# Kernel tuning notes

Hardware: AMD Instinct MI355X
Metric: run time of the kernel (lower is better)

The kernel has to match this reference:

```python
import jax, jax.numpy as jnp
import numpy as np

B, T, C = 2, 2048, 1024
E = 1024          # total attention embedding (head_size arg of TransformerBlock)
H = 16            # n_heads
HS = E // H       # per-head size = 64
FF = 4 * C        # ffwd_mul * in_embd
EPS = 1e-5


def setup_inputs() -> dict:
    key = jax.random.key(0)
    ks = jax.random.split(key, 20)
    s = lambda fan_in: 1.0 / np.sqrt(fan_in)
    return {
        "x":     jax.random.normal(ks[0], (B, T, C), jnp.float32),
        "Wq":    jax.random.normal(ks[1], (C, E), jnp.float32) * s(C),
        "bq":    jnp.zeros((E,), jnp.float32),
        "Wk":    jax.random.normal(ks[2], (C, E), jnp.float32) * s(C),
        "bk":    jnp.zeros((E,), jnp.float32),
        "Wv":    jax.random.normal(ks[3], (C, E), jnp.float32) * s(C),
        "bv":    jnp.zeros((E,), jnp.float32),
        "Wo":    jax.random.normal(ks[4], (E, C), jnp.float32) * s(E),
        "bo":    jnp.zeros((C,), jnp.float32),
        "ln1_g": jnp.ones((C,), jnp.float32),
        "ln1_b": jnp.zeros((C,), jnp.float32),
        "W1":    jax.random.normal(ks[5], (C, FF), jnp.float32) * s(C),
        "b1":    jnp.zeros((FF,), jnp.float32),
        "W2":    jax.random.normal(ks[6], (FF, C), jnp.float32) * s(FF),
        "b2":    jnp.zeros((C,), jnp.float32),
        "ln2_g": jnp.ones((C,), jnp.float32),
        "ln2_b": jnp.zeros((C,), jnp.float32),
        "Wc":    jax.random.normal(ks[7], (C, C), jnp.float32) * s(C),
        "bc":    jnp.zeros((C,), jnp.float32),
    }


def _layernorm(x, g, b):
    mu = jnp.mean(x, axis=-1, keepdims=True)
    var = jnp.mean(jnp.square(x - mu), axis=-1, keepdims=True)
    return (x - mu) * jax.lax.rsqrt(var + EPS) * g + b


def _attention(x, Wq, bq, Wk, bk, Wv, bv, Wo, bo):
    # batched equivalent of the per-head Linear q/k/v loop + concat
    q = (x @ Wq + bq).reshape(B, T, H, HS)
    k = (x @ Wk + bk).reshape(B, T, H, HS)
    v = (x @ Wv + bv).reshape(B, T, H, HS)
    scores = jnp.einsum("bthd,bshd->bhts", q, k) / np.sqrt(HS)  # no causal mask in source
    wei = jax.nn.softmax(scores, axis=-1)
    out = jnp.einsum("bhts,bshd->bthd", wei, v).reshape(B, T, E)
    return out @ Wo + bo


def reference(x, Wq, bq, Wk, bk, Wv, bv, Wo, bo, ln1_g, ln1_b,
              W1, b1, W2, b2, ln2_g, ln2_b, Wc, bc):
    out = _layernorm(x + _attention(x, Wq, bq, Wk, bk, Wv, bv, Wo, bo), ln1_g, ln1_b)
    ff = jax.nn.gelu(out @ W1 + b1, approximate=False) @ W2 + b2  # torch GELU is exact erf
    out = _layernorm(out + ff, ln2_g, ln2_b)
    # Conv1d(C, C, kernel_size=1) over transposed input == pointwise linear
    out = out @ Wc.T + bc
    return out
```

## Files before the change

kernel.cpp:

```cpp
#include <hip/hip_runtime.h>
#include <hip/hip_bf16.h>
#include <cstdint>
#include <cstddef>

#define DEVINL __device__ __forceinline__

typedef __attribute__((ext_vector_type(4)))  float f32x4;
typedef __attribute__((ext_vector_type(16))) float f32x16;
typedef __attribute__((ext_vector_type(8)))  short s16x8;

#define QSCALE 0.1803368801111204f

DEVINL short f2bf(float f) {
  union { float f; unsigned u; } v; v.f = f;
  unsigned r = (v.u + 0x7fffu + ((v.u >> 16) & 1u)) >> 16;
  return (short)r;
}

DEVINL void gload_lds16(const void* g, void* l) {
  __builtin_amdgcn_global_load_lds((const __attribute__((address_space(1))) void*)g,
                                   (__attribute__((address_space(3))) void*)l,
                                   16, 0, 0);
}

DEVINL s16x8 lds_frag(const short* base, int row, int cb) {
  const int addr = row * 128 + (cb ^ ((row & 7) << 4));
  return *(const s16x8*)((const char*)base + addr);
}

enum { EPI_F32 = 0, EPI_GELU = 1, EPI_RES = 2, EPI_QKV = 3 };

template <int EPI, int BM>
__global__ __launch_bounds__(256) void gemm_bt(
    const short* __restrict__ A, const short* __restrict__ Bt,
    const float* __restrict__ bias, const float* __restrict__ res,
    float* __restrict__ outF, short* __restrict__ outB,
    short* __restrict__ qp, short* __restrict__ kp, short* __restrict__ vt,
    int M, int N, int K)
{
  constexpr int MI = BM / 32;
  constexpr int CAW = BM / 64;
  __shared__ short As[2][BM * 32];
  __shared__ short Bs[2][128 * 32];
  const int tid = threadIdx.x;
  const int w = tid >> 6, lane = tid & 63;
  const int wr = w >> 1, wc = w & 1;

  const int gx = gridDim.x;
  int id = blockIdx.x + gx * blockIdx.y;
  const int cpx = (gx * gridDim.y) >> 3;
  id = (id & 7) * cpx + (id >> 3);
  const int n0 = (id % gx) * 128, m0 = (id / gx) * BM;

  const int lrow = lane >> 2, lk = (lane & 3) << 3;
  const short* Ag = A + (size_t)m0 * K;
  const short* Bg = Bt + (size_t)n0 * K;

#define GSTAGE(kk, bufi)                                                     \
  {                                                                          \
    _Pragma("unroll") for (int i = 0; i < CAW; ++i) {                        \
      const int c = w * CAW + i;                                             \
      gload_lds16(Ag + (size_t)(c * 16 + lrow) * K + ((kk) + lk),            \
                  &As[bufi][c * 512]);                                       \
    }                                                                        \
    _Pragma("unroll") for (int i = 0; i < 2; ++i) {                          \
      const int c = w * 2 + i;                                               \
      gload_lds16(Bg + (size_t)(c * 16 + lrow) * K + ((kk) + lk),            \
                  &Bs[bufi][c * 512]);                                       \
    }                                                                        \
  }

  f32x4 acc[MI][4] = {};

  GSTAGE(0, 0);
  __syncthreads();
  int cur = 0;

  for (int kk = 0; kk < K; kk += 32) {
    if (kk + 32 < K) GSTAGE(kk + 32, cur ^ 1);
    s16x8 af[MI], bf[4];
#pragma unroll
    for (int mi = 0; mi < MI; ++mi)
      af[mi] = *(const s16x8*)&As[cur][(wr * (BM / 2) + mi * 16 + (lane & 15)) * 32 + ((lane >> 4) << 3)];
#pragma unroll
    for (int ni = 0; ni < 4; ++ni)
      bf[ni] = *(const s16x8*)&Bs[cur][(wc * 64 + ni * 16 + (lane & 15)) * 32 + ((lane >> 4) << 3)];
    __builtin_amdgcn_s_setprio(1);
#pragma unroll
    for (int mi = 0; mi < MI; ++mi)
#pragma unroll
      for (int ni = 0; ni < 4; ++ni)
        acc[mi][ni] = __builtin_amdgcn_mfma_f32_16x16x32_bf16(af[mi], bf[ni], acc[mi][ni], 0, 0, 0);
    __builtin_amdgcn_s_setprio(0);
    __syncthreads();
    cur ^= 1;
  }
#undef GSTAGE

  const int rbase = m0 + wr * (BM / 2) + ((lane >> 4) << 2);
  const int cbase = n0 + wc * 64 + (lane & 15);
#pragma unroll
  for (int mi = 0; mi < MI; ++mi) {
#pragma unroll
    for (int ni = 0; ni < 4; ++ni) {
      const int col = cbase + ni * 16;
      const float bv = bias[col];
      if (EPI == EPI_QKV) {
        const int e = col & 1023, id3 = col >> 10;
        const int h = e >> 6, d = e & 63;
        const int row0 = rbase + mi * 16;
        const int b = row0 >> 11, t0 = row0 & 2047;
        if (id3 == 0) {
#pragma unroll
          for (int j = 0; j < 4; ++j)
            qp[((size_t)(b * 16 + h) * 2048 + t0 + j) * 64 + d] = f2bf((acc[mi][ni][j] + bv) * QSCALE);
        } else if (id3 == 1) {
#pragma unroll
          for (int j = 0; j < 4; ++j)
            kp[((size_t)(b * 16 + h) * 2048 + t0 + j) * 64 + d] = f2bf(acc[mi][ni][j] + bv);
        } else {
          short4 pk4;
          pk4.x = f2bf(acc[mi][ni][0] + bv); pk4.y = f2bf(acc[mi][ni][1] + bv);
          pk4.z = f2bf(acc[mi][ni][2] + bv); pk4.w = f2bf(acc[mi][ni][3] + bv);
          *(short4*)&vt[((size_t)(b * 16 + h) * 64 + d) * 2048 + t0] = pk4;
        }
      } else {
#pragma unroll
        for (int j = 0; j < 4; ++j) {
          const int row = rbase + mi * 16 + j;
          float v = acc[mi][ni][j] + bv;
          if (EPI == EPI_GELU) {
            outB[(size_t)row * N + col] = f2bf(0.5f * v * (1.0f + erff(v * 0.70710678118654752f)));
          } else if (EPI == EPI_RES) {
            outF[(size_t)row * N + col] = v + res[(size_t)row * N + col];
          } else {
            outF[(size_t)row * N + col] = v;
          }
        }
      }
    }
  }
}

__global__ __launch_bounds__(256) void attn_kernel(
    const short* __restrict__ qg, const short* __restrict__ kg,
    const short* __restrict__ vtg, short* __restrict__ outB)
{
  __shared__ short Ks[2][64 * 64];
  __shared__ short Vs[2][64 * 64];
  __shared__ float sbuf[4][32];

  const int bh = blockIdx.x, qb = blockIdx.y;
  const int tid = threadIdx.x, w = tid >> 6, lane = tid & 63;
  const int b = bh >> 4, h = bh & 15;
  const int ql = lane & 31, hi = lane >> 5;
  const int qrow = qb * 128 + w * 32 + ql;

  s16x8 qf[4];
  const short* qrp = qg + ((size_t)bh * 2048 + qrow) * 64;
#pragma unroll
  for (int kd = 0; kd < 4; ++kd)
    qf[kd] = *(const s16x8*)(qrp + kd * 16 + hi * 8);

  f32x16 o[2] = {};
  float mrow = -3.0e38f, lsum = 0.f;

  const size_t kbase = (size_t)bh * 2048 * 64;
  const size_t vbase = (size_t)bh * 64 * 2048;

#define STAGE(t, bufi)                                                         \
  {                                                                            \
    _Pragma("unroll") for (int i = 0; i < 2; ++i) {                            \
      const int pb = i * 4096 + w * 1024;                                      \
      const int p = pb + lane * 16;                                            \
      const int row = p >> 7;                                                  \
      const int cs = (p & 127) ^ ((row & 7) << 4);                             \
      gload_lds16(kg + kbase + (size_t)((t) * 64 + row) * 64 + (cs >> 1),      \
                  &Ks[bufi][pb >> 1]);                                         \
      gload_lds16(vtg + vbase + (size_t)row * 2048 + (t) * 64 + (cs >> 1),     \
                  &Vs[bufi][pb >> 1]);                                         \
    }                                                                          \
  }

  STAGE(0, 0);
  __syncthreads();

  for (int t = 0; t < 32; ++t) {
    const int buf = t & 1;
    if (t < 31) STAGE(t + 1, buf ^ 1);
    const short* kb = Ks[buf];
    const short* vb = Vs[buf];

    f32x16 pS[2] = {};
    __builtin_amdgcn_s_setprio(1);
#pragma unroll
    for (int kd = 0; kd < 4; ++kd) {
      const s16x8 a0 = lds_frag(kb, ql,      kd * 32 + hi * 16);
      const s16x8 a1 = lds_frag(kb, 32 + ql, kd * 32 + hi * 16);
      pS[0] = __builtin_amdgcn_mfma_f32_32x32x16_bf16(a0, qf[kd], pS[0], 0, 0, 0);
      pS[1] = __builtin_amdgcn_mfma_f32_32x32x16_bf16(a1, qf[kd], pS[1], 0, 0, 0);
    }
    __builtin_amdgcn_s_setprio(0);

    float pm = pS[0][0];
#pragma unroll
    for (int r = 1; r < 16; ++r) pm = fmaxf(pm, pS[0][r]);
#pragma unroll
    for (int r = 0; r < 16; ++r) pm = fmaxf(pm, pS[1][r]);
    pm = fmaxf(pm, __shfl_xor(pm, 32));

    if (!__all(pm <= mrow + 8.0f)) {
      const float mnew = fmaxf(mrow, pm);
      const float alpha = exp2f(mrow - mnew);
      mrow = mnew;
      lsum *= alpha;
      sbuf[w][ql] = alpha;
#pragma unroll
      for (int r = 0; r < 16; ++r) {
        const float a = sbuf[w][(r & 3) + 8 * (r >> 2) + 4 * hi];
        o[0][r] *= a; o[1][r] *= a;
      }
    }

    float rs = 0.f;
#pragma unroll
    for (int r = 0; r < 16; ++r) { pS[0][r] = exp2f(pS[0][r] - mrow); rs += pS[0][r]; }
#pragma unroll
    for (int r = 0; r < 16; ++r) { pS[1][r] = exp2f(pS[1][r] - mrow); rs += pS[1][r]; }
    rs += __shfl_xor(rs, 32);
    lsum += rs;

#pragma unroll
    for (int ks = 0; ks < 4; ++ks) {
      const int tI = ks >> 1, b8 = (ks & 1) * 8;
      unsigned u0, u1, v0, v1;
      asm("v_cvt_pk_bf16_f32 %0, %1, %2" : "=v"(u0) : "v"(pS[tI][b8 + 0]), "v"(pS[tI][b8 + 1]));
      asm("v_cvt_pk_bf16_f32 %0, %1, %2" : "=v"(u1) : "v"(pS[tI][b8 + 2]), "v"(pS[tI][b8 + 3]));
      asm("v_cvt_pk_bf16_f32 %0, %1, %2" : "=v"(v0) : "v"(pS[tI][b8 + 4]), "v"(pS[tI][b8 + 5]));
      asm("v_cvt_pk_bf16_f32 %0, %1, %2" : "=v"(v1) : "v"(pS[tI][b8 + 6]), "v"(pS[tI][b8 + 7]));
      const unsigned su0 = (unsigned)__shfl_xor((int)u0, 32);
      const unsigned su1 = (unsigned)__shfl_xor((int)u1, 32);
      const unsigned sv0 = (unsigned)__shfl_xor((int)v0, 32);
      const unsigned sv1 = (unsigned)__shfl_xor((int)v1, 32);
      union { unsigned u[4]; s16x8 s; } pa;
      pa.u[0] = hi ? sv0 : u0;
      pa.u[1] = hi ? sv1 : u1;
      pa.u[2] = hi ? v0 : su0;
      pa.u[3] = hi ? v1 : su1;
      const s16x8 vf0 = lds_frag(vb, ql,      ks * 32 + hi * 16);
      const s16x8 vf1 = lds_frag(vb, 32 + ql, ks * 32 + hi * 16);
      __builtin_amdgcn_s_setprio(1);
      o[0] = __builtin_amdgcn_mfma_f32_32x32x16_bf16(pa.s, vf0, o[0], 0, 0, 0);
      o[1] = __builtin_amdgcn_mfma_f32_32x32x16_bf16(pa.s, vf1, o[1], 0, 0, 0);
      __builtin_amdgcn_s_setprio(0);
    }
    __syncthreads();
  }

  sbuf[w][ql] = lsum;
#pragma unroll
  for (int r = 0; r < 16; ++r) {
    const int q = (r & 3) + 8 * (r >> 2) + 4 * hi;
    const float linv = 1.0f / sbuf[w][q];
    const int tq = qb * 128 + w * 32 + q;
    const size_t orow = ((size_t)b * 2048 + tq) * 1024 + h * 64;
    outB[orow + ql]      = f2bf(o[0][r] * linv);
    outB[orow + 32 + ql] = f2bf(o[1][r] * linv);
  }
}

__global__ __launch_bounds__(256) void ln_kernel(
    const float* in, float* outF, short* __restrict__ outB,
    const float* __restrict__ gw, const float* __restrict__ bw)
{
  const int row = blockIdx.x, tid = threadIdx.x;
  const float4 v = ((const float4*)(in + (size_t)row * 1024))[tid];
  float s = v.x + v.y + v.z + v.w;
  float s2 = v.x * v.x + v.y * v.y + v.z * v.z + v.w * v.w;
#pragma unroll
  for (int m = 1; m < 64; m <<= 1) { s += __shfl_xor(s, m); s2 += __shfl_xor(s2, m); }
  __shared__ float as1[4], as2[4];
  if ((tid & 63) == 0) { as1[tid >> 6] = s; as2[tid >> 6] = s2; }
  __syncthreads();
  s = as1[0] + as1[1] + as1[2] + as1[3];
  s2 = as2[0] + as2[1] + as2[2] + as2[3];
  const float mu = s * (1.f / 1024.f);
  const float var = s2 * (1.f / 1024.f) - mu * mu;
  const float rstd = rsqrtf(var + 1e-5f);
  const float4 g = ((const float4*)gw)[tid];
  const float4 bb = ((const float4*)bw)[tid];
  float4 y;
  y.x = (v.x - mu) * rstd * g.x + bb.x;
  y.y = (v.y - mu) * rstd * g.y + bb.y;
  y.z = (v.z - mu) * rstd * g.z + bb.z;
  y.w = (v.w - mu) * rstd * g.w + bb.w;
  ((float4*)(outF + (size_t)row * 1024))[tid] = y;
  short4 ob; ob.x = f2bf(y.x); ob.y = f2bf(y.y); ob.z = f2bf(y.z); ob.w = f2bf(y.w);
  ((short4*)(outB + (size_t)row * 1024))[tid] = ob;
}

__global__ __launch_bounds__(256) void transpose_cast(
    const float* __restrict__ src, short* __restrict__ dst, int R, int Cc)
{
  __shared__ float tile[32][33];
  const int c0 = blockIdx.x * 32, r0 = blockIdx.y * 32;
  const int x = threadIdx.x & 31, y = threadIdx.x >> 5;
#pragma unroll
  for (int i = 0; i < 32; i += 8)
    tile[y + i][x] = src[(size_t)(r0 + y + i) * Cc + c0 + x];
  __syncthreads();
#pragma unroll
  for (int i = 0; i < 32; i += 8)
    dst[(size_t)(c0 + y + i) * R + r0 + x] = f2bf(tile[x][y + i]);
}

__global__ __launch_bounds__(256) void cast_bf16_kernel(
    const float* __restrict__ src, short* __restrict__ dst, int n4)
{
  const int i = blockIdx.x * 256 + threadIdx.x;
  if (i < n4) {
    const float4 v = ((const float4*)src)[i];
    short4 o; o.x = f2bf(v.x); o.y = f2bf(v.y); o.z = f2bf(v.z); o.w = f2bf(v.w);
    ((short4*)dst)[i] = o;
  }
}

__global__ void concat3_kernel(const float* a, const float* b, const float* c, float* o)
{
  const int i = blockIdx.x * 256 + threadIdx.x;
  if (i < 3072) o[i] = (i < 1024 ? a[i] : (i < 2048 ? b[i - 1024] : c[i - 2048]));
}

extern "C" void kernel_launch(void* const* d_in, const int* in_sizes, int n_in,
                              void* d_out, int out_size, void* d_ws, size_t ws_size,
                              hipStream_t stream)
{
  const float* x    = (const float*)d_in[0];
  const float* Wq   = (const float*)d_in[1];
  const float* bq   = (const float*)d_in[2];
  const float* Wk   = (const float*)d_in[3];
  const float* bk   = (const float*)d_in[4];
  const float* Wv   = (const float*)d_in[5];
  const float* bv   = (const float*)d_in[6];
  const float* Wo   = (const float*)d_in[7];
  const float* bo   = (const float*)d_in[8];
  const float* ln1g = (const float*)d_in[9];
  const float* ln1b = (const float*)d_in[10];
  const float* W1   = (const float*)d_in[11];
  const float* b1   = (const float*)d_in[12];
  const float* W2   = (const float*)d_in[13];
  const float* b2   = (const float*)d_in[14];
  const float* ln2g = (const float*)d_in[15];
  const float* ln2b = (const float*)d_in[16];
  const float* Wc   = (const float*)d_in[17];
  const float* bc   = (const float*)d_in[18];
  float* out = (float*)d_out;

  char* p = (char*)d_ws;
  auto alloc = [&](size_t bytes) { char* r = p; p += (bytes + 255) & ~(size_t)255; return r; };

  short* qkvT = (short*)alloc((size_t)3072 * 1024 * 2);
  short* WoT  = (short*)alloc((size_t)1024 * 1024 * 2);
  short* W1T  = (short*)alloc((size_t)4096 * 1024 * 2);
  short* W2T  = (short*)alloc((size_t)1024 * 4096 * 2);
  short* WcB  = (short*)alloc((size_t)1024 * 1024 * 2);
  float* bqkv = (float*)alloc(3072 * 4);
  short* xb   = (short*)alloc((size_t)4096 * 1024 * 2);
  short* qb_  = (short*)alloc((size_t)32 * 2048 * 64 * 2);
  short* kb_  = (short*)alloc((size_t)32 * 2048 * 64 * 2);
  short* vt_  = (short*)alloc((size_t)32 * 64 * 2048 * 2);
  short* ff1  = xb;
  short* attnO= (short*)alloc((size_t)4096 * 1024 * 2);
  float* h1   = (float*)alloc((size_t)4096 * 1024 * 4);
  short* o1b  = (short*)alloc((size_t)4096 * 1024 * 2);
  float* h2   = (float*)alloc((size_t)4096 * 1024 * 4);
  short* o2b  = (short*)alloc((size_t)4096 * 1024 * 2);

  cast_bf16_kernel<<<4096, 256, 0, stream>>>(x, xb, 1048576);
  transpose_cast<<<dim3(32, 32),  256, 0, stream>>>(Wq, qkvT,                1024, 1024);
  transpose_cast<<<dim3(32, 32),  256, 0, stream>>>(Wk, qkvT + 1024 * 1024,  1024, 1024);
  transpose_cast<<<dim3(32, 32),  256, 0, stream>>>(Wv, qkvT + 2048 * 1024,  1024, 1024);
  transpose_cast<<<dim3(32, 32),  256, 0, stream>>>(Wo, WoT,                 1024, 1024);
  transpose_cast<<<dim3(128, 32), 256, 0, stream>>>(W1, W1T,                 1024, 4096);
  transpose_cast<<<dim3(32, 128), 256, 0, stream>>>(W2, W2T,                 4096, 1024);
  cast_bf16_kernel<<<1024, 256, 0, stream>>>(Wc, WcB, 262144);
  concat3_kernel<<<12, 256, 0, stream>>>(bq, bk, bv, bqkv);

  gemm_bt<EPI_QKV, 128><<<dim3(24, 32), 256, 0, stream>>>(
      xb, qkvT, bqkv, nullptr, nullptr, nullptr, qb_, kb_, vt_, 4096, 3072, 1024);
  attn_kernel<<<dim3(32, 16), 256, 0, stream>>>(qb_, kb_, vt_, attnO);
  gemm_bt<EPI_RES, 64><<<dim3(8, 64), 256, 0, stream>>>(
      attnO, WoT, bo, x, h1, nullptr, nullptr, nullptr, nullptr, 4096, 1024, 1024);
  ln_kernel<<<4096, 256, 0, stream>>>(h1, h1, o1b, ln1g, ln1b);
  gemm_bt<EPI_GELU, 128><<<dim3(32, 32), 256, 0, stream>>>(
      o1b, W1T, b1, nullptr, nullptr, ff1, nullptr, nullptr, nullptr, 4096, 4096, 1024);
  gemm_bt<EPI_RES, 64><<<dim3(8, 64), 256, 0, stream>>>(
      ff1, W2T, b2, h1, h2, nullptr, nullptr, nullptr, nullptr, 4096, 1024, 4096);
  ln_kernel<<<4096, 256, 0, stream>>>(h2, h2, o2b, ln2g, ln2b);
  gemm_bt<EPI_F32, 64><<<dim3(8, 64), 256, 0, stream>>>(
      o2b, WcB, bc, nullptr, out, nullptr, nullptr, nullptr, nullptr, 4096, 1024, 1024);
}
```

Measured before the change: 454.6 us.

## Split attention over key halves with log-sum-exp combine; fuse prep kernels

Splits the attention kernel's key/value sequence into two halves along a new grid dimension (flash-decoding style). Each half writes a normalized bf16 partial output plus a per-row log-sum-exp, and a new combine kernel merges the two. This doubles the attention grid from 512 to 1024 blocks so more CUs are busy. It also merges the nine weight cast/transpose/concat launches into a single prep kernel to cut launch overhead. The cost is extra traffic for the partials and combine, plus an extra bf16 rounding of the partial outputs.

```diff
diff --git a/kernel.cpp b/kernel.cpp
--- a/kernel.cpp
+++ b/kernel.cpp
@@ -15,6 +15,10 @@
   union { float f; unsigned u; } v; v.f = f;
   unsigned r = (v.u + 0x7fffu + ((v.u >> 16) & 1u)) >> 16;
   return (short)r;
+}
+DEVINL float bf2f(short s) {
+  union { unsigned u; float f; } v; v.u = ((unsigned)(unsigned short)s) << 16;
+  return v.f;
 }
 
 DEVINL void gload_lds16(const void* g, void* l) {
@@ -144,13 +148,14 @@
 
 __global__ __launch_bounds__(256) void attn_kernel(
     const short* __restrict__ qg, const short* __restrict__ kg,
-    const short* __restrict__ vtg, short* __restrict__ outB)
+    const short* __restrict__ vtg, short* __restrict__ part,
+    float* __restrict__ Lst)
 {
   __shared__ short Ks[2][64 * 64];
   __shared__ short Vs[2][64 * 64];
   __shared__ float sbuf[4][32];
 
-  const int bh = blockIdx.x, qb = blockIdx.y;
+  const int bh = blockIdx.x, qb = blockIdx.y, ks2 = blockIdx.z;
   const int tid = threadIdx.x, w = tid >> 6, lane = tid & 63;
   const int b = bh >> 4, h = bh & 15;
   const int ql = lane & 31, hi = lane >> 5;
@@ -165,8 +170,9 @@
   f32x16 o[2] = {};
   float mrow = -3.0e38f, lsum = 0.f;
 
-  const size_t kbase = (size_t)bh * 2048 * 64;
+  const size_t kbase = (size_t)bh * 2048 * 64 + (size_t)ks2 * 1024 * 64;
   const size_t vbase = (size_t)bh * 64 * 2048;
+  const int scol0 = ks2 * 1024;
 
 #define STAGE(t, bufi)                                                         \
   {                                                                            \
@@ -177,7 +183,7 @@
       const int cs = (p & 127) ^ ((row & 7) << 4);                             \
       gload_lds16(kg + kbase + (size_t)((t) * 64 + row) * 64 + (cs >> 1),      \
                   &Ks[bufi][pb >> 1]);                                         \
-      gload_lds16(vtg + vbase + (size_t)row * 2048 + (t) * 64 + (cs >> 1),     \
+      gload_lds16(vtg + vbase + (size_t)row * 2048 + scol0 + (t) * 64 + (cs >> 1), \
                   &Vs[bufi][pb >> 1]);                                         \
     }                                                                          \
   }
@@ -185,9 +191,9 @@
   STAGE(0, 0);
   __syncthreads();
 
-  for (int t = 0; t < 32; ++t) {
+  for (int t = 0; t < 16; ++t) {
     const int buf = t & 1;
-    if (t < 31) STAGE(t + 1, buf ^ 1);
+    if (t < 15) STAGE(t + 1, buf ^ 1);
     const short* kb = Ks[buf];
     const short* vb = Vs[buf];
 
@@ -257,16 +263,45 @@
     __syncthreads();
   }
 
+  short* po = part + (size_t)ks2 * (4096 * 1024);
   sbuf[w][ql] = lsum;
+  if (hi == 0)
+    Lst[ks2 * 65536 + bh * 2048 + qb * 128 + w * 32 + ql] = mrow + log2f(lsum);
 #pragma unroll
   for (int r = 0; r < 16; ++r) {
     const int q = (r & 3) + 8 * (r >> 2) + 4 * hi;
     const float linv = 1.0f / sbuf[w][q];
     const int tq = qb * 128 + w * 32 + q;
     const size_t orow = ((size_t)b * 2048 + tq) * 1024 + h * 64;
-    outB[orow + ql]      = f2bf(o[0][r] * linv);
-    outB[orow + 32 + ql] = f2bf(o[1][r] * linv);
-  }
+    po[orow + ql]      = f2bf(o[0][r] * linv);
+    po[orow + 32 + ql] = f2bf(o[1][r] * linv);
+  }
+}
+
+__global__ __launch_bounds__(256) void attn_combine(
+    const short* __restrict__ part, const float* __restrict__ Lst,
+    short* __restrict__ outB)
+{
+  const int gid = blockIdx.x * 256 + threadIdx.x;
+  const int row = gid >> 7;
+  const int wi = gid & 127;
+  const int h = wi >> 3, d8 = (wi & 7) * 8;
+  const int b = row >> 11, t = row & 2047;
+  const int bh = b * 16 + h;
+  const float L0 = Lst[bh * 2048 + t];
+  const float L1 = Lst[65536 + bh * 2048 + t];
+  const float mx = fmaxf(L0, L1);
+  const float w0 = exp2f(L0 - mx), w1 = exp2f(L1 - mx);
+  const float inv = 1.f / (w0 + w1);
+  const float a0 = w0 * inv, a1 = w1 * inv;
+  const size_t off = (size_t)row * 1024 + h * 64 + d8;
+  const s16x8 p0 = *(const s16x8*)&part[off];
+  const s16x8 p1 = *(const s16x8*)&part[(size_t)4096 * 1024 + off];
+  s16x8 ov;
+#pragma unroll
+  for (int e = 0; e < 8; ++e)
+    ov[e] = f2bf(a0 * bf2f(p0[e]) + a1 * bf2f(p1[e]));
+  *(s16x8*)&outB[off] = ov;
 }
 
 __global__ __launch_bounds__(256) void ln_kernel(
@@ -299,36 +334,53 @@
   ((short4*)(outB + (size_t)row * 1024))[tid] = ob;
 }
 
-__global__ __launch_bounds__(256) void transpose_cast(
-    const float* __restrict__ src, short* __restrict__ dst, int R, int Cc)
+__global__ __launch_bounds__(256) void prep_kernel(
+    const float* __restrict__ x,  const float* __restrict__ Wq,
+    const float* __restrict__ Wk, const float* __restrict__ Wv,
+    const float* __restrict__ Wo, const float* __restrict__ W1,
+    const float* __restrict__ W2, const float* __restrict__ Wc,
+    const float* __restrict__ bq, const float* __restrict__ bk,
+    const float* __restrict__ bv,
+    short* __restrict__ xb, short* __restrict__ qkvT, short* __restrict__ WoT,
+    short* __restrict__ W1T, short* __restrict__ W2T, short* __restrict__ WcB,
+    float* __restrict__ bqkv)
 {
   __shared__ float tile[32][33];
-  const int c0 = blockIdx.x * 32, r0 = blockIdx.y * 32;
-  const int x = threadIdx.x & 31, y = threadIdx.x >> 5;
+  const int bid = blockIdx.x, tid = threadIdx.x;
+  const float* tsrc = nullptr; short* tdst = nullptr;
+  const float* csrc = nullptr; short* cdst = nullptr;
+  int R = 0, Cc = 0, tb = 0, cb = 0;
+  if (bid < 4096)        { csrc = x;  cdst = xb;  cb = bid; }
+  else if (bid < 5120)   { tsrc = Wq; tdst = qkvT;           R = 1024; Cc = 1024; tb = bid - 4096; }
+  else if (bid < 6144)   { tsrc = Wk; tdst = qkvT + 1048576; R = 1024; Cc = 1024; tb = bid - 5120; }
+  else if (bid < 7168)   { tsrc = Wv; tdst = qkvT + 2097152; R = 1024; Cc = 1024; tb = bid - 6144; }
+  else if (bid < 8192)   { tsrc = Wo; tdst = WoT;            R = 1024; Cc = 1024; tb = bid - 7168; }
+  else if (bid < 12288)  { tsrc = W1; tdst = W1T;            R = 1024; Cc = 4096; tb = bid - 8192; }
+  else if (bid < 16384)  { tsrc = W2; tdst = W2T;            R = 4096; Cc = 1024; tb = bid - 12288; }
+  else if (bid < 17408)  { csrc = Wc; cdst = WcB; cb = bid - 16384; }
+  else {
+    const int i = (bid - 17408) * 256 + tid;
+    if (i < 3072) bqkv[i] = (i < 1024 ? bq[i] : (i < 2048 ? bk[i - 1024] : bv[i - 2048]));
+    return;
+  }
+  if (csrc) {
+    const int i = cb * 256 + tid;
+    const float4 v = ((const float4*)csrc)[i];
+    short4 oq; oq.x = f2bf(v.x); oq.y = f2bf(v.y); oq.z = f2bf(v.z); oq.w = f2bf(v.w);
+    ((short4*)cdst)[i] = oq;
+    return;
+  }
+  const int xtiles = Cc >> 5;
+  const int bx = tb % xtiles, by = tb / xtiles;
+  const int c0 = bx * 32, r0 = by * 32;
+  const int xx = tid & 31, yy = tid >> 5;
 #pragma unroll
   for (int i = 0; i < 32; i += 8)
-    tile[y + i][x] = src[(size_t)(r0 + y + i) * Cc + c0 + x];
+    tile[yy + i][xx] = tsrc[(size_t)(r0 + yy + i) * Cc + c0 + xx];
   __syncthreads();
 #pragma unroll
   for (int i = 0; i < 32; i += 8)
-    dst[(size_t)(c0 + y + i) * R + r0 + x] = f2bf(tile[x][y + i]);
-}
-
-__global__ __launch_bounds__(256) void cast_bf16_kernel(
-    const float* __restrict__ src, short* __restrict__ dst, int n4)
-{
-  const int i = blockIdx.x * 256 + threadIdx.x;
-  if (i < n4) {
-    const float4 v = ((const float4*)src)[i];
-    short4 o; o.x = f2bf(v.x); o.y = f2bf(v.y); o.z = f2bf(v.z); o.w = f2bf(v.w);
-    ((short4*)dst)[i] = o;
-  }
-}
-
-__global__ void concat3_kernel(const float* a, const float* b, const float* c, float* o)
-{
-  const int i = blockIdx.x * 256 + threadIdx.x;
-  if (i < 3072) o[i] = (i < 1024 ? a[i] : (i < 2048 ? b[i - 1024] : c[i - 2048]));
+    tdst[(size_t)(c0 + yy + i) * R + r0 + xx] = f2bf(tile[xx][yy + i]);
 }
 
 extern "C" void kernel_launch(void* const* d_in, const int* in_sizes, int n_in,
@@ -376,19 +428,17 @@
   float* h2   = (float*)alloc((size_t)4096 * 1024 * 4);
   short* o2b  = (short*)alloc((size_t)4096 * 1024 * 2);
 
-  cast_bf16_kernel<<<4096, 256, 0, stream>>>(x, xb, 1048576);
-  transpose_cast<<<dim3(32, 32),  256, 0, stream>>>(Wq, qkvT,                1024, 1024);
-  transpose_cast<<<dim3(32, 32),  256, 0, stream>>>(Wk, qkvT + 1024 * 1024,  1024, 1024);
-  transpose_cast<<<dim3(32, 32),  256, 0, stream>>>(Wv, qkvT + 2048 * 1024,  1024, 1024);
-  transpose_cast<<<dim3(32, 32),  256, 0, stream>>>(Wo, WoT,                 1024, 1024);
-  transpose_cast<<<dim3(128, 32), 256, 0, stream>>>(W1, W1T,                 1024, 4096);
-  transpose_cast<<<dim3(32, 128), 256, 0, stream>>>(W2, W2T,                 4096, 1024);
-  cast_bf16_kernel<<<1024, 256, 0, stream>>>(Wc, WcB, 262144);
-  concat3_kernel<<<12, 256, 0, stream>>>(bq, bk, bv, bqkv);
+  short* part = (short*)h1;
+  float* Lst  = (float*)h2;
+
+  prep_kernel<<<17420, 256, 0, stream>>>(x, Wq, Wk, Wv, Wo, W1, W2, Wc,
+                                         bq, bk, bv,
+                                         xb, qkvT, WoT, W1T, W2T, WcB, bqkv);
 
   gemm_bt<EPI_QKV, 128><<<dim3(24, 32), 256, 0, stream>>>(
       xb, qkvT, bqkv, nullptr, nullptr, nullptr, qb_, kb_, vt_, 4096, 3072, 1024);
-  attn_kernel<<<dim3(32, 16), 256, 0, stream>>>(qb_, kb_, vt_, attnO);
+  attn_kernel<<<dim3(32, 16, 2), 256, 0, stream>>>(qb_, kb_, vt_, part, Lst);
+  attn_combine<<<2048, 256, 0, stream>>>(part, Lst, attnO);
   gemm_bt<EPI_RES, 64><<<dim3(8, 64), 256, 0, stream>>>(
       attnO, WoT, bo, x, h1, nullptr, nullptr, nullptr, nullptr, 4096, 1024, 1024);
   ln_kernel<<<4096, 256, 0, stream>>>(h1, h1, o1b, ln1g, ln1b);
```

Result: faster. 443.9 us (-2.3%).
